# Performance work log

Hardware: AMD Instinct MI355X
Metric: run time of the kernel (lower is better)

The kernel has to match this reference:

```python
import jax, jax.numpy as jnp
import numpy as np

CHANNELS = 256
LAYERS = 4
IN_FEAT = 118
N_NODES = 20000
N_EDGES = 320000


def setup_inputs() -> dict:
    key = jax.random.key(0)
    ks = jax.random.split(key, 4 + 4 * LAYERS)
    x = jax.random.normal(ks[0], (N_NODES, IN_FEAT), dtype=jnp.float32)
    edge_index = jax.random.randint(ks[1], (2, N_EDGES), 0, N_NODES, dtype=jnp.int64)
    s = 1.0 / np.sqrt(CHANNELS)
    W_embed = jax.random.normal(ks[2], (IN_FEAT, CHANNELS), dtype=jnp.float32) / np.sqrt(IN_FEAT)
    b_embed = jnp.zeros((CHANNELS,), dtype=jnp.float32)
    W1 = jax.random.normal(ks[3], (LAYERS, CHANNELS, CHANNELS), dtype=jnp.float32) * s
    b1 = jnp.zeros((LAYERS, CHANNELS), dtype=jnp.float32)
    W2 = jax.random.normal(ks[4], (LAYERS, CHANNELS, CHANNELS), dtype=jnp.float32) * s
    b2 = jnp.zeros((LAYERS, CHANNELS), dtype=jnp.float32)
    return {"x": x, "edge_index": edge_index, "W_embed": W_embed, "b_embed": b_embed,
            "W1": W1, "b1": b1, "W2": W2, "b2": b2}


def reference(x, edge_index, W_embed, b_embed, W1, b1, W2, b2):
    n = x.shape[0]
    src, dst = edge_index[0], edge_index[1]
    # in-degree for mean aggregation (constant across layers)
    cnt = jax.ops.segment_sum(jnp.ones(src.shape[0], dtype=x.dtype), dst, num_segments=n)
    inv_cnt = (1.0 / jnp.maximum(cnt, 1.0))[:, None]
    h = x @ W_embed + b_embed  # [N, C]
    for l in range(W1.shape[0]):
        # message: gather source features, dense + exact GELU (dropout off in eval)
        msg = jax.nn.gelu(h[src] @ W1[l] + b1[l], approximate=False)  # [E, C]
        # mean-scatter aggregate over destination nodes
        agg = jax.ops.segment_sum(msg, dst, num_segments=n) * inv_cnt  # [N, C]
        # update: dense + GELU
        h = jax.nn.gelu(agg @ W2[l] + b2[l], approximate=False)
    return jnp.mean(h, axis=1)  # [N]
```

## Files before the change

### kernel.cpp

```cpp
#include <hip/hip_runtime.h>
#include <math.h>
#include <stdint.h>

#define CH 256

typedef _Float16 half8 __attribute__((ext_vector_type(8)));
typedef _Float16 half4 __attribute__((ext_vector_type(4)));
typedef _Float16 half2v __attribute__((ext_vector_type(2)));
typedef float f32x4 __attribute__((ext_vector_type(4)));

__device__ __forceinline__ float gelu_exact(float v) {
    return 0.5f * v * (1.0f + erff(v * 0.70710678118654752f));
}

__device__ __forceinline__ float acc_pk(uint32_t u, float acc) {
    half2v h = __builtin_bit_cast(half2v, u);
#if __has_builtin(__builtin_amdgcn_fdot2)
    half2v ones = {(_Float16)1.0f, (_Float16)1.0f};
    return __builtin_amdgcn_fdot2(h, ones, acc, false);
#else
    return acc + (float)h.x + (float)h.y;
#endif
}

__global__ void wsplit_kernel(const float* __restrict__ W1, const float* __restrict__ W2,
                              _Float16* __restrict__ WThi, _Float16* __restrict__ WTlo) {
    int idx = blockIdx.x * blockDim.x + threadIdx.x;
    int n   = idx & 255;
    int kg  = (idx >> 8) & 31;
    int mat = idx >> 13;
    const float* W = (mat < 4) ? (W1 + (size_t)mat * 65536)
                               : (W2 + (size_t)(mat - 4) * 65536);
    _Float16 hi[8], lo[8];
#pragma unroll
    for (int j = 0; j < 8; j++) {
        float v = W[(size_t)(kg * 8 + j) * CH + n];
        _Float16 h = (_Float16)v;
        hi[j] = h;
        lo[j] = (_Float16)(v - (float)h);
    }
    size_t off = (size_t)mat * 65536 + ((size_t)(kg >> 2) * 256 + n) * 32 + (kg & 3) * 8;
    *(half8*)(WThi + off) = *(half8*)&hi[0];
    *(half8*)(WTlo + off) = *(half8*)&lo[0];
}

__global__ void wesplit_kernel(const float* __restrict__ We,
                               _Float16* __restrict__ WeTh, _Float16* __restrict__ WeTl) {
    int idx = blockIdx.x * blockDim.x + threadIdx.x;
    if (idx >= 4096) return;
    int n  = idx >> 4;
    int k8 = (idx & 15) * 8;
    _Float16 hi[8], lo[8];
#pragma unroll
    for (int j = 0; j < 8; j++) {
        int k = k8 + j;
        float v = (k < 118) ? We[(size_t)k * CH + n] : 0.f;
        _Float16 h = (_Float16)v;
        hi[j] = h;
        lo[j] = (_Float16)(v - (float)h);
    }
    size_t off = ((size_t)(k8 >> 5) * 256 + n) * 32 + (k8 & 31);
    *(half8*)(WeTh + off) = *(half8*)&hi[0];
    *(half8*)(WeTl + off) = *(half8*)&lo[0];
}

__global__ void xsplit_kernel(const float* __restrict__ x,
                              _Float16* __restrict__ xh, _Float16* __restrict__ xl,
                              int N, int Mpad) {
    int idx = blockIdx.x * blockDim.x + threadIdx.x;
    int n  = idx >> 4;
    int c8 = (idx & 15) * 8;
    if (n >= N) return;
    _Float16 hi[8], lo[8];
#pragma unroll
    for (int j = 0; j < 8; j++) {
        int c = c8 + j;
        float v = (c < 118) ? x[(size_t)n * 118 + c] : 0.f;
        _Float16 h = (_Float16)v;
        hi[j] = h;
        lo[j] = (_Float16)(v - (float)h);
    }
    size_t off = ((size_t)(c8 >> 5) * Mpad + n) * 32 + (c8 & 31);
    *(half8*)(xh + off) = *(half8*)&hi[0];
    *(half8*)(xl + off) = *(half8*)&lo[0];
}

template<int KT, bool DOGELU, bool TILED>
__global__ __launch_bounds__(256, 4) void mgemm_kernel(
    const _Float16* __restrict__ Ah_g, const _Float16* __restrict__ Al_g,
    const _Float16* __restrict__ Bh_g, const _Float16* __restrict__ Bl_g,
    const float* __restrict__ bias,
    _Float16* __restrict__ Oh, _Float16* __restrict__ Ol,
    int Mpad, int MC)
{
    __shared__ __align__(16) char smem[30720];
    _Float16 (*Ah)[40] = (_Float16(*)[40])smem;
    _Float16 (*Al)[40] = (_Float16(*)[40])(smem + 10240);
    _Float16 (*Bh)[40] = (_Float16(*)[40])(smem + 20480);
    _Float16 (*Bl)[40] = (_Float16(*)[40])(smem + 25600);
    uint32_t (*Obuf)[68] = (uint32_t(*)[68])smem;

    int b    = blockIdx.x;
    int xcd  = b & 7;
    int slot = b >> 3;
    int mt   = xcd * MC + (slot >> 2);
    int nt   = slot & 3;
    if (mt * 128 >= Mpad) return;
    int m0 = mt * 128;
    int n0 = nt * 64;

    int tid  = threadIdx.x;
    int lane = tid & 63;
    int wave = tid >> 6;
    int wr = wave >> 1;
    int wc = wave & 1;

    f32x4 acc[4][2];
#pragma unroll
    for (int i = 0; i < 4; i++)
#pragma unroll
        for (int j = 0; j < 2; j++) acc[i][j] = (f32x4){0.f, 0.f, 0.f, 0.f};

    const int Lb    = tid * 8;
    const int arow0 = Lb >> 5;
    const int ak    = Lb & 31;

    for (int kt = 0; kt < KT; kt++) {
        const _Float16* pah = Ah_g + ((size_t)kt * Mpad + m0) * 32;
        const _Float16* pal = Al_g + ((size_t)kt * Mpad + m0) * 32;
        const _Float16* pbh = Bh_g + ((size_t)kt * 256 + n0) * 32;
        const _Float16* pbl = Bl_g + ((size_t)kt * 256 + n0) * 32;
        half8 a0 = *(const half8*)(pah + Lb);
        half8 a1 = *(const half8*)(pah + 2048 + Lb);
        half8 a2 = *(const half8*)(pal + Lb);
        half8 a3 = *(const half8*)(pal + 2048 + Lb);
        half8 b0 = *(const half8*)(pbh + Lb);
        half8 b1 = *(const half8*)(pbl + Lb);
        *(half8*)&Ah[arow0][ak]      = a0;
        *(half8*)&Ah[64 + arow0][ak] = a1;
        *(half8*)&Al[arow0][ak]      = a2;
        *(half8*)&Al[64 + arow0][ak] = a3;
        *(half8*)&Bh[arow0][ak]      = b0;
        *(half8*)&Bl[arow0][ak]      = b1;
        __syncthreads();

        {
            int frow = lane & 15;
            int fk   = (lane >> 4) * 8;
            half8 ah[4], al[4], bh[2], bl[2];
#pragma unroll
            for (int rf = 0; rf < 4; rf++) {
                int r = wr * 64 + rf * 16 + frow;
                ah[rf] = *(const half8*)&Ah[r][fk];
                al[rf] = *(const half8*)&Al[r][fk];
            }
#pragma unroll
            for (int cf = 0; cf < 2; cf++) {
                int c = wc * 32 + cf * 16 + frow;
                bh[cf] = *(const half8*)&Bh[c][fk];
                bl[cf] = *(const half8*)&Bl[c][fk];
            }
#pragma unroll
            for (int rf = 0; rf < 4; rf++)
#pragma unroll
                for (int cf = 0; cf < 2; cf++) {
                    acc[rf][cf] = __builtin_amdgcn_mfma_f32_16x16x32_f16(ah[rf], bh[cf], acc[rf][cf], 0, 0, 0);
                    acc[rf][cf] = __builtin_amdgcn_mfma_f32_16x16x32_f16(ah[rf], bl[cf], acc[rf][cf], 0, 0, 0);
                    acc[rf][cf] = __builtin_amdgcn_mfma_f32_16x16x32_f16(al[rf], bh[cf], acc[rf][cf], 0, 0, 0);
                }
        }
        __syncthreads();
    }

    int ccol = lane & 15;
    int crow = (lane >> 4) * 4;
    float bb[2];
    bb[0] = bias[n0 + wc * 32 + ccol];
    bb[1] = bias[n0 + wc * 32 + 16 + ccol];
#pragma unroll
    for (int half = 0; half < 2; half++) {
        if (wr == half) {
#pragma unroll
            for (int cf = 0; cf < 2; cf++)
#pragma unroll
                for (int rf = 0; rf < 4; rf++)
#pragma unroll
                    for (int q = 0; q < 4; q++) {
                        float v = acc[rf][cf][q] + bb[cf];
                        float g = DOGELU ? gelu_exact(v) : v;
                        _Float16 hi = (_Float16)g;
                        _Float16 lo = (_Float16)(g - (float)hi);
                        uint32_t u = (uint32_t)__builtin_bit_cast(uint16_t, hi)
                                   | ((uint32_t)__builtin_bit_cast(uint16_t, lo) << 16);
                        Obuf[rf * 16 + crow + q][wc * 32 + cf * 16 + ccol] = u;
                    }
        }
        __syncthreads();
#pragma unroll
        for (int i = 0; i < 8; i++) {
            int idx = i * 512 + tid * 2;
            int row = idx >> 6;
            int c   = idx & 63;
            uint32_t u0 = Obuf[row][c];
            uint32_t u1 = Obuf[row][c + 1];
            int grow = m0 + half * 64 + row;
            int gcol = n0 + c;
            if (TILED) {
                uint32_t hi2 = (u0 & 0xffffu) | (u1 << 16);
                uint32_t lo2 = (u0 >> 16) | (u1 & 0xffff0000u);
                size_t off = ((size_t)(gcol >> 5) * Mpad + grow) * 32 + (gcol & 31);
                *(uint32_t*)(Oh + off) = hi2;
                *(uint32_t*)(Ol + off) = lo2;
            } else {
                uint2 pk; pk.x = u0; pk.y = u1;
                *(uint2*)((uint32_t*)Oh + (size_t)grow * CH + gcol) = pk;
            }
        }
        __syncthreads();
    }
}

__global__ void zero_int_kernel(int* p, int n) {
    int i = blockIdx.x * blockDim.x + threadIdx.x;
    if (i < n) p[i] = 0;
}

__global__ void degree_kernel(const int* __restrict__ ei, int E, int* deg) {
    int e = blockIdx.x * blockDim.x + threadIdx.x;
    if (e < E) atomicAdd(&deg[ei[E + e]], 1);
}

__global__ void scan_part_kernel(const int* __restrict__ deg, int* bsum, int N) {
    int t = threadIdx.x;
    int base = blockIdx.x * 1024 + t * 4;
    int4 v = {0, 0, 0, 0};
    if (base + 3 < N) v = *(const int4*)(deg + base);
    else {
        if (base + 0 < N) v.x = deg[base + 0];
        if (base + 1 < N) v.y = deg[base + 1];
        if (base + 2 < N) v.z = deg[base + 2];
        if (base + 3 < N) v.w = deg[base + 3];
    }
    __shared__ int sh[256];
    sh[t] = v.x + v.y + v.z + v.w;
    __syncthreads();
    for (int off = 128; off; off >>= 1) {
        if (t < off) sh[t] += sh[t + off];
        __syncthreads();
    }
    if (t == 0) bsum[blockIdx.x] = sh[0];
}

__global__ void scan_top_kernel(const int* __restrict__ bsum, int* boff, int B) {
    __shared__ int sh[256];
    int t = threadIdx.x;
    int own = (t < B) ? bsum[t] : 0;
    sh[t] = own;
    __syncthreads();
    for (int off = 1; off < 256; off <<= 1) {
        int v = (t >= off) ? sh[t - off] : 0;
        __syncthreads();
        sh[t] += v;
        __syncthreads();
    }
    if (t < B) boff[t] = sh[t] - own;
}

__global__ void scan_final_kernel(const int* __restrict__ deg, const int* __restrict__ boff,
                                  int* row_ptr, int* fill_pos, float* inv, int N, int E) {
    int t = threadIdx.x;
    int base = blockIdx.x * 1024 + t * 4;
    int4 v = {0, 0, 0, 0};
    if (base + 3 < N) v = *(const int4*)(deg + base);
    else {
        if (base + 0 < N) v.x = deg[base + 0];
        if (base + 1 < N) v.y = deg[base + 1];
        if (base + 2 < N) v.z = deg[base + 2];
        if (base + 3 < N) v.w = deg[base + 3];
    }
    int own = v.x + v.y + v.z + v.w;
    __shared__ int sh[256];
    sh[t] = own;
    __syncthreads();
    for (int off = 1; off < 256; off <<= 1) {
        int s = (t >= off) ? sh[t - off] : 0;
        __syncthreads();
        sh[t] += s;
        __syncthreads();
    }
    int run = boff[blockIdx.x] + (sh[t] - own);
    int4 rp;
    rp.x = run;
    rp.y = run + v.x;
    rp.z = rp.y + v.y;
    rp.w = rp.z + v.z;
    if (base + 3 < N) {
        *(int4*)(row_ptr + base) = rp;
        *(int4*)(fill_pos + base) = rp;
        float4 iv;
        iv.x = 1.0f / fmaxf((float)v.x, 1.0f);
        iv.y = 1.0f / fmaxf((float)v.y, 1.0f);
        iv.z = 1.0f / fmaxf((float)v.z, 1.0f);
        iv.w = 1.0f / fmaxf((float)v.w, 1.0f);
        *(float4*)(inv + base) = iv;
    } else {
        int rr[4] = {rp.x, rp.y, rp.z, rp.w};
        int dd[4] = {v.x, v.y, v.z, v.w};
        for (int q = 0; q < 4; q++) {
            if (base + q < N) {
                row_ptr[base + q] = rr[q];
                fill_pos[base + q] = rr[q];
                inv[base + q] = 1.0f / fmaxf((float)dd[q], 1.0f);
            }
        }
    }
    if (blockIdx.x == 0 && t == 0) row_ptr[N] = E;
}

__global__ void fill_kernel(const int* __restrict__ ei, int E, int* fill_pos, int* colv) {
    int e = blockIdx.x * blockDim.x + threadIdx.x;
    if (e < E) {
        int p = atomicAdd(&fill_pos[ei[E + e]], 1);
        colv[p] = ei[e];
    }
}

__global__ __launch_bounds__(256) void agg_kernel(
    const uint32_t* __restrict__ tpk,
    const int* __restrict__ row_ptr, const int* __restrict__ colv,
    const float* __restrict__ inv,
    _Float16* __restrict__ aggh, _Float16* __restrict__ aggl,
    int N, int Mpad)
{
    int b = blockIdx.x;
    int slice = b & 7;
    int n = (b >> 3) * 16 + (threadIdx.x >> 4);
    if (n >= N) return;
    int lane = threadIdx.x & 15;
    const uint32_t* base = tpk + slice * 32 + lane * 2;

    int s = row_ptr[n], e = row_ptr[n + 1];
    float e0 = 0.f, o0 = 0.f, e1 = 0.f, o1 = 0.f;
    int j = s;
    for (; j + 4 <= e; j += 4) {
        int c0 = colv[j], c1 = colv[j + 1], c2 = colv[j + 2], c3 = colv[j + 3];
        uint2 u0 = *(const uint2*)(base + (size_t)c0 * CH);
        uint2 u1 = *(const uint2*)(base + (size_t)c1 * CH);
        uint2 u2 = *(const uint2*)(base + (size_t)c2 * CH);
        uint2 u3 = *(const uint2*)(base + (size_t)c3 * CH);
        e0 = acc_pk(u0.x, e0); o0 = acc_pk(u0.y, o0);
        e1 = acc_pk(u1.x, e1); o1 = acc_pk(u1.y, o1);
        e0 = acc_pk(u2.x, e0); o0 = acc_pk(u2.y, o0);
        e1 = acc_pk(u3.x, e1); o1 = acc_pk(u3.y, o1);
    }
    for (; j < e; j++) {
        uint2 u = *(const uint2*)(base + (size_t)colv[j] * CH);
        e0 = acc_pk(u.x, e0); o0 = acc_pk(u.y, o0);
    }
    float sc = inv[n];
    float v0 = (e0 + e1) * sc;
    float v1 = (o0 + o1) * sc;
    _Float16 h0 = (_Float16)v0, h1 = (_Float16)v1;
    half2v oh = {h0, h1};
    half2v ol = {(_Float16)(v0 - (float)h0), (_Float16)(v1 - (float)h1)};
    size_t ooff = ((size_t)slice * Mpad + n) * 32 + lane * 2;
    *(half2v*)(aggh + ooff) = oh;
    *(half2v*)(aggl + ooff) = ol;
}

__global__ void mean_kernel(const _Float16* __restrict__ hh, const _Float16* __restrict__ hl,
                            float* __restrict__ out, int N, int Mpad) {
    int n = blockIdx.x * 4 + (threadIdx.x >> 6);
    if (n >= N) return;
    int lane = threadIdx.x & 63;
    size_t off = ((size_t)(lane >> 3) * Mpad + n) * 32 + ((lane * 4) & 31);
    half4 vh = *(const half4*)(hh + off);
    half4 vl = *(const half4*)(hl + off);
    float s = 0.f;
#pragma unroll
    for (int q = 0; q < 4; q++) s += (float)vh[q] + (float)vl[q];
#pragma unroll
    for (int off2 = 32; off2; off2 >>= 1) s += __shfl_down(s, off2, 64);
    if (lane == 0) out[n] = s * (1.0f / 256.0f);
}

extern "C" void kernel_launch(void* const* d_in, const int* in_sizes, int n_in,
                              void* d_out, int out_size, void* d_ws, size_t ws_size,
                              hipStream_t stream) {
    const float* x       = (const float*)d_in[0];
    const int*   ei      = (const int*)d_in[1];
    const float* W_embed = (const float*)d_in[2];
    const float* b_embed = (const float*)d_in[3];
    const float* W1      = (const float*)d_in[4];
    const float* b1      = (const float*)d_in[5];
    const float* W2      = (const float*)d_in[6];
    const float* b2      = (const float*)d_in[7];
    float* out = (float*)d_out;

    int N = in_sizes[0] / 118;
    int E = in_sizes[1] / 2;
    int SB = (N + 1023) / 1024;
    int Mpad = ((N + 127) / 128) * 128;
    size_t NC = (size_t)Mpad * CH;

    _Float16* hh   = (_Float16*)d_ws;
    _Float16* hl   = hh + NC;
    _Float16* th   = hl + NC;
    _Float16* tl   = th + NC;
    _Float16* ah   = tl + NC;
    _Float16* al   = ah + NC;
    _Float16* WThi = al + NC;
    _Float16* WTlo = WThi + 8 * 65536;
    _Float16* WeTh = WTlo + 8 * 65536;
    _Float16* WeTl = WeTh + 32768;
    float*    inv      = (float*)(WeTl + 32768);
    int*      deg      = (int*)(inv + N);
    int*      row_ptr  = deg + N;
    int*      fill_pos = row_ptr + (N + 1);
    int*      colv     = fill_pos + N;
    int*      bsum     = colv + E;
    int*      boff     = bsum + 256;

    uint32_t* tpk = (uint32_t*)th;
    _Float16* xh = th;
    _Float16* xl = th + (size_t)Mpad * 128;

    zero_int_kernel<<<(N + 255) / 256, 256, 0, stream>>>(deg, N);
    degree_kernel<<<(E + 255) / 256, 256, 0, stream>>>(ei, E, deg);
    scan_part_kernel<<<SB, 256, 0, stream>>>(deg, bsum, N);
    scan_top_kernel<<<1, 256, 0, stream>>>(bsum, boff, SB);
    scan_final_kernel<<<SB, 256, 0, stream>>>(deg, boff, row_ptr, fill_pos, inv, N, E);
    fill_kernel<<<(E + 255) / 256, 256, 0, stream>>>(ei, E, fill_pos, colv);
    wsplit_kernel<<<256, 256, 0, stream>>>(W1, W2, WThi, WTlo);
    wesplit_kernel<<<16, 256, 0, stream>>>(W_embed, WeTh, WeTl);
    xsplit_kernel<<<(N * 16 + 255) / 256, 256, 0, stream>>>(x, xh, xl, N, Mpad);

    int mtiles = Mpad / 128;
    int MC = (mtiles + 7) / 8;
    int mgrid = 8 * MC * 4;
    int agrid = 8 * ((N + 15) / 16);

    mgemm_kernel<4, false, true><<<mgrid, 256, 0, stream>>>(xh, xl, WeTh, WeTl, b_embed,
                                                            hh, hl, Mpad, MC);
    for (int l = 0; l < 4; l++) {
        mgemm_kernel<8, true, false><<<mgrid, 256, 0, stream>>>(hh, hl,
                                                                WThi + (size_t)l * 65536,
                                                                WTlo + (size_t)l * 65536,
                                                                b1 + (size_t)l * CH,
                                                                (_Float16*)tpk, nullptr,
                                                                Mpad, MC);
        agg_kernel<<<agrid, 256, 0, stream>>>(tpk, row_ptr, colv, inv, ah, al, N, Mpad);
        mgemm_kernel<8, true, true><<<mgrid, 256, 0, stream>>>(ah, al,
                                                               WThi + (size_t)(4 + l) * 65536,
                                                               WTlo + (size_t)(4 + l) * 65536,
                                                               b2 + (size_t)l * CH,
                                                               hh, hl, Mpad, MC);
    }
    mean_kernel<<<(N + 3) / 4, 256, 0, stream>>>(hh, hl, out, N, Mpad);
}
```

Measured before the change: 406.4 us.

## Preload full B panel to LDS and stream A fragments directly from global

The GEMM kernel now loads the whole 64-column B slice (all K tiles) into shared memory once, then reads A fragments straight from global memory into registers with a fully unrolled K loop. This removes the per-K-tile LDS staging of A and the two barriers per iteration. In exchange, LDS use grows with KT, and launch bounds drop to 2 blocks per SM, which lowers occupancy. The direct global A loads are not shared across waves, so some A data is fetched twice (wc=0/1). The epilogue buffer now aliases the B panel, which may be too small for some KT.

```diff
diff --git a/kernel.cpp b/kernel.cpp
--- a/kernel.cpp
+++ b/kernel.cpp
@@ -86,19 +86,16 @@
 }
 
 template<int KT, bool DOGELU, bool TILED>
-__global__ __launch_bounds__(256, 4) void mgemm_kernel(
+__global__ __launch_bounds__(256, 2) void mgemm_kernel(
     const _Float16* __restrict__ Ah_g, const _Float16* __restrict__ Al_g,
     const _Float16* __restrict__ Bh_g, const _Float16* __restrict__ Bl_g,
     const float* __restrict__ bias,
     _Float16* __restrict__ Oh, _Float16* __restrict__ Ol,
     int Mpad, int MC)
 {
-    __shared__ __align__(16) char smem[30720];
-    _Float16 (*Ah)[40] = (_Float16(*)[40])smem;
-    _Float16 (*Al)[40] = (_Float16(*)[40])(smem + 10240);
-    _Float16 (*Bh)[40] = (_Float16(*)[40])(smem + 20480);
-    _Float16 (*Bl)[40] = (_Float16(*)[40])(smem + 25600);
-    uint32_t (*Obuf)[68] = (uint32_t(*)[68])smem;
+    const int BST = KT * 32 + 8;
+    __shared__ _Float16 Bh_s[64][KT * 32 + 8];
+    __shared__ _Float16 Bl_s[64][KT * 32 + 8];
 
     int b    = blockIdx.x;
     int xcd  = b & 7;
@@ -115,63 +112,55 @@
     int wr = wave >> 1;
     int wc = wave & 1;
 
+    {
+        const int CH8 = KT * 4;
+        for (int i = tid; i < 64 * CH8; i += 256) {
+            int c   = i / CH8;
+            int kc8 = (i % CH8) * 8;
+            int kt_ = kc8 >> 5, kw = kc8 & 31;
+            size_t src = ((size_t)kt_ * 256 + (n0 + c)) * 32 + kw;
+            *(half8*)&Bh_s[c][kc8] = *(const half8*)(Bh_g + src);
+            *(half8*)&Bl_s[c][kc8] = *(const half8*)(Bl_g + src);
+        }
+    }
+    __syncthreads();
+
     f32x4 acc[4][2];
 #pragma unroll
     for (int i = 0; i < 4; i++)
 #pragma unroll
         for (int j = 0; j < 2; j++) acc[i][j] = (f32x4){0.f, 0.f, 0.f, 0.f};
 
-    const int Lb    = tid * 8;
-    const int arow0 = Lb >> 5;
-    const int ak    = Lb & 31;
-
+    int frow = lane & 15;
+    int fk   = (lane >> 4) * 8;
+
+#pragma unroll
     for (int kt = 0; kt < KT; kt++) {
-        const _Float16* pah = Ah_g + ((size_t)kt * Mpad + m0) * 32;
-        const _Float16* pal = Al_g + ((size_t)kt * Mpad + m0) * 32;
-        const _Float16* pbh = Bh_g + ((size_t)kt * 256 + n0) * 32;
-        const _Float16* pbl = Bl_g + ((size_t)kt * 256 + n0) * 32;
-        half8 a0 = *(const half8*)(pah + Lb);
-        half8 a1 = *(const half8*)(pah + 2048 + Lb);
-        half8 a2 = *(const half8*)(pal + Lb);
-        half8 a3 = *(const half8*)(pal + 2048 + Lb);
-        half8 b0 = *(const half8*)(pbh + Lb);
-        half8 b1 = *(const half8*)(pbl + Lb);
-        *(half8*)&Ah[arow0][ak]      = a0;
-        *(half8*)&Ah[64 + arow0][ak] = a1;
-        *(half8*)&Al[arow0][ak]      = a2;
-        *(half8*)&Al[64 + arow0][ak] = a3;
-        *(half8*)&Bh[arow0][ak]      = b0;
-        *(half8*)&Bl[arow0][ak]      = b1;
-        __syncthreads();
-
-        {
-            int frow = lane & 15;
-            int fk   = (lane >> 4) * 8;
-            half8 ah[4], al[4], bh[2], bl[2];
-#pragma unroll
-            for (int rf = 0; rf < 4; rf++) {
-                int r = wr * 64 + rf * 16 + frow;
-                ah[rf] = *(const half8*)&Ah[r][fk];
-                al[rf] = *(const half8*)&Al[r][fk];
+        half8 ah[4], al[4], bh[2], bl[2];
+#pragma unroll
+        for (int rf = 0; rf < 4; rf++) {
+            size_t ro = ((size_t)kt * Mpad + (m0 + wr * 64 + rf * 16 + frow)) * 32 + fk;
+            ah[rf] = *(const half8*)(Ah_g + ro);
+            al[rf] = *(const half8*)(Al_g + ro);
+        }
+#pragma unroll
+        for (int cf = 0; cf < 2; cf++) {
+            int c = wc * 32 + cf * 16 + frow;
+            bh[cf] = *(const half8*)&Bh_s[c][kt * 32 + fk];
+            bl[cf] = *(const half8*)&Bl_s[c][kt * 32 + fk];
+        }
+#pragma unroll
+        for (int rf = 0; rf < 4; rf++)
+#pragma unroll
+            for (int cf = 0; cf < 2; cf++) {
+                acc[rf][cf] = __builtin_amdgcn_mfma_f32_16x16x32_f16(ah[rf], bh[cf], acc[rf][cf], 0, 0, 0);
+                acc[rf][cf] = __builtin_amdgcn_mfma_f32_16x16x32_f16(ah[rf], bl[cf], acc[rf][cf], 0, 0, 0);
+                acc[rf][cf] = __builtin_amdgcn_mfma_f32_16x16x32_f16(al[rf], bh[cf], acc[rf][cf], 0, 0, 0);
             }
-#pragma unroll
-            for (int cf = 0; cf < 2; cf++) {
-                int c = wc * 32 + cf * 16 + frow;
-                bh[cf] = *(const half8*)&Bh[c][fk];
-                bl[cf] = *(const half8*)&Bl[c][fk];
-            }
-#pragma unroll
-            for (int rf = 0; rf < 4; rf++)
-#pragma unroll
-                for (int cf = 0; cf < 2; cf++) {
-                    acc[rf][cf] = __builtin_amdgcn_mfma_f32_16x16x32_f16(ah[rf], bh[cf], acc[rf][cf], 0, 0, 0);
-                    acc[rf][cf] = __builtin_amdgcn_mfma_f32_16x16x32_f16(ah[rf], bl[cf], acc[rf][cf], 0, 0, 0);
-                    acc[rf][cf] = __builtin_amdgcn_mfma_f32_16x16x32_f16(al[rf], bh[cf], acc[rf][cf], 0, 0, 0);
-                }
-        }
-        __syncthreads();
-    }
-
+    }
+    __syncthreads();
+
+    uint32_t (*Obuf)[68] = (uint32_t(*)[68])&Bh_s[0][0];
     int ccol = lane & 15;
     int crow = (lane >> 4) * 4;
     float bb[2];
```

After: 574.2 us. +41.3%, slower.
